# Kernel optimization log

Measured on AMD Instinct MI355X. Metric: run time of the kernel, lower is better.

## Reference

```python
import jax, jax.numpy as jnp
import numpy as np

N_STATE = 1280
N_HEAD = 20
D_HEAD = N_STATE // N_HEAD  # 64
N_MLP = 4 * N_STATE         # 5120
EPS = 1e-5


def _layer_norm(x, gamma, beta):
    mu = jnp.mean(x, axis=-1, keepdims=True)
    var = jnp.mean(jnp.square(x - mu), axis=-1, keepdims=True)
    return (x - mu) * jax.lax.rsqrt(var + EPS) * gamma + beta


def setup_inputs() -> dict:
    key = jax.random.key(0)
    ks = jax.random.split(key, 16)
    s = lambda fan_in: 1.0 / np.sqrt(fan_in)
    d = {
        "x": jax.random.normal(ks[0], (1, 1500, N_STATE), jnp.float32),
        # attention projections (stored [in, out]; torch Linear does x @ W.T + b)
        "Wq": jax.random.normal(ks[1], (N_STATE, N_STATE), jnp.float32) * s(N_STATE),
        "bq": jax.random.normal(ks[2], (N_STATE,), jnp.float32) * 0.02,
        "Wk": jax.random.normal(ks[3], (N_STATE, N_STATE), jnp.float32) * s(N_STATE),  # no bias
        "Wv": jax.random.normal(ks[4], (N_STATE, N_STATE), jnp.float32) * s(N_STATE),
        "bv": jax.random.normal(ks[5], (N_STATE,), jnp.float32) * 0.02,
        "Wo": jax.random.normal(ks[6], (N_STATE, N_STATE), jnp.float32) * s(N_STATE),
        "bo": jax.random.normal(ks[7], (N_STATE,), jnp.float32) * 0.02,
        # layer norms
        "ln1_g": jnp.ones((N_STATE,), jnp.float32),
        "ln1_b": jnp.zeros((N_STATE,), jnp.float32),
        "ln2_g": jnp.ones((N_STATE,), jnp.float32),
        "ln2_b": jnp.zeros((N_STATE,), jnp.float32),
        # MLP
        "W1": jax.random.normal(ks[8], (N_STATE, N_MLP), jnp.float32) * s(N_STATE),
        "b1": jax.random.normal(ks[9], (N_MLP,), jnp.float32) * 0.02,
        "W2": jax.random.normal(ks[10], (N_MLP, N_STATE), jnp.float32) * s(N_MLP),
        "b2": jax.random.normal(ks[11], (N_STATE,), jnp.float32) * 0.02,
    }
    return d


def reference(x, Wq, bq, Wk, Wv, bv, Wo, bo, ln1_g, ln1_b, ln2_g, ln2_b, W1, b1, W2, b2):
    B, S, C = x.shape
    scale = D_HEAD ** -0.5

    # --- multi-head self-attention ---
    h = _layer_norm(x, ln1_g, ln1_b)
    q = (h @ Wq + bq).reshape(B, S, N_HEAD, D_HEAD)
    k = (h @ Wk).reshape(B, S, N_HEAD, D_HEAD)
    v = (h @ Wv + bv).reshape(B, S, N_HEAD, D_HEAD)
    # scores: [B, H, Q, K]; softmax over keys (dim=1 'k' in the torch einsum)
    scores = jnp.einsum('bqhd,bkhd->bhqk', q, k) * scale
    w = jax.nn.softmax(scores, axis=-1)
    attn = jnp.einsum('bhqk,bkhd->bqhd', w, v).reshape(B, S, C)
    attn = attn @ Wo + bo
    x = x + attn

    # --- MLP (exact GELU, matching torch nn.GELU default) ---
    h2 = _layer_norm(x, ln2_g, ln2_b)
    h2 = jax.nn.gelu(h2 @ W1 + b1, approximate=False)
    x = x + (h2 @ W2 + b2)
    return x
```

## Files before the change

kernel.cpp:

```cpp
#include <hip/hip_runtime.h>
#include <hip/hip_bf16.h>
#include <math.h>

typedef __bf16 bf16x8 __attribute__((ext_vector_type(8)));
typedef float f32x4 __attribute__((ext_vector_type(4)));

#define SEQ 1500
#define CDIM 1280
#define NHEAD 20
#define DHEAD 64
#define NMLP 5120
#define QKVN 3840
#define VTLD 1504
#define APAD 68

#define GLOAD_LDS16(gp, lp)                                                    \
  __builtin_amdgcn_global_load_lds(                                            \
      (const __attribute__((address_space(1))) unsigned int*)(gp),             \
      (__attribute__((address_space(3))) unsigned int*)(lp), 16, 0, 0)

__global__ void detect_kernel(const unsigned int* __restrict__ xw,
                              int* __restrict__ flag) {
  __shared__ int cnt[256];
  const unsigned int w = xw[threadIdx.x];
  const unsigned int e = (w >> 7) & 0xFF;
  cnt[threadIdx.x] = (e >= 100 && e <= 150) ? 1 : 0;
  __syncthreads();
  for (int s = 128; s > 0; s >>= 1) {
    if (threadIdx.x < (unsigned)s) cnt[threadIdx.x] += cnt[threadIdx.x + s];
    __syncthreads();
  }
  if (threadIdx.x == 0) flag[0] = (cnt[0] >= 160) ? 1 : 0;
}

__global__ __launch_bounds__(256) void pack_params_kernel(
    const void* bq, const void* bv, const void* bo, const void* g1,
    const void* be1, const void* g2, const void* be2, const void* b1,
    const void* b2, __bf16* __restrict__ pb, const int* __restrict__ flag) {
  const int isbf = flag[0];
  const int i = blockIdx.x * 256 + threadIdx.x;
  if (i >= 16640) return;
  auto ld = [&](const void* p, int j) -> float {
    return isbf ? (float)((const __bf16*)p)[j] : ((const float*)p)[j];
  };
  float v;
  if (i < 3840) {
    if (i < 1280) v = ld(bq, i);
    else if (i < 2560) v = 0.f;
    else v = ld(bv, i - 2560);
  } else if (i < 5120) v = ld(bo, i - 3840);
  else if (i < 6400) v = ld(g1, i - 5120);
  else if (i < 7680) v = ld(be1, i - 6400);
  else if (i < 8960) v = ld(g2, i - 7680);
  else if (i < 10240) v = ld(be2, i - 8960);
  else if (i < 15360) v = ld(b1, i - 10240);
  else v = ld(b2, i - 15360);
  pb[i] = (__bf16)v;
}

__device__ __forceinline__ void transpose_body(const void* in, __bf16* out,
                                               int K, int N, int isbf) {
  __shared__ __bf16 t[32][33];
  const int tx = threadIdx.x, ty = threadIdx.y;
  const int n0 = blockIdx.x * 32, k0 = blockIdx.y * 32;
  if (isbf) {
    const __bf16* s = (const __bf16*)in;
#pragma unroll
    for (int i = ty; i < 32; i += 8)
      t[i][tx] = s[(size_t)(k0 + i) * N + n0 + tx];
  } else {
    const float* s = (const float*)in;
#pragma unroll
    for (int i = ty; i < 32; i += 8)
      t[i][tx] = (__bf16)s[(size_t)(k0 + i) * N + n0 + tx];
  }
  __syncthreads();
#pragma unroll
  for (int i = ty; i < 32; i += 8)
    out[(size_t)(n0 + i) * K + k0 + tx] = t[tx][i];
}

__global__ __launch_bounds__(256) void transpose_kernel(const void* __restrict__ in,
                                                        __bf16* __restrict__ out,
                                                        int K, int N,
                                                        const int* __restrict__ flag) {
  transpose_body(in, out, K, N, flag[0]);
}

__global__ __launch_bounds__(256) void transpose3_kernel(const void* __restrict__ Wq,
                                                         const void* __restrict__ Wk,
                                                         const void* __restrict__ Wv,
                                                         __bf16* __restrict__ out,
                                                         const int* __restrict__ flag) {
  const void* in = blockIdx.z == 0 ? Wq : (blockIdx.z == 1 ? Wk : Wv);
  transpose_body(in, out + (size_t)blockIdx.z * CDIM * CDIM, CDIM, CDIM, flag[0]);
}

__global__ __launch_bounds__(256) void transpose_act_kernel(const __bf16* __restrict__ in,
                                                            __bf16* __restrict__ out,
                                                            int istride) {
  __shared__ __bf16 t[32][33];
  const int tx = threadIdx.x, ty = threadIdx.y;
  const int n0 = blockIdx.x * 32, k0 = blockIdx.y * 32;
#pragma unroll
  for (int i = ty; i < 32; i += 8) {
    const int k = k0 + i;
    t[i][tx] = (k < SEQ) ? in[(size_t)k * istride + n0 + tx] : (__bf16)0.f;
  }
  __syncthreads();
#pragma unroll
  for (int i = ty; i < 32; i += 8) {
    const int kk = k0 + tx;
    if (kk < VTLD) out[(size_t)(n0 + i) * VTLD + kk] = t[tx][i];
  }
}

__global__ __launch_bounds__(256) void ln_kernel(const void* __restrict__ X,
                                                 const __bf16* __restrict__ gamma,
                                                 const __bf16* __restrict__ beta,
                                                 __bf16* __restrict__ Y,
                                                 int xflag, const int* __restrict__ flag) {
  const int isf32 = xflag ? (flag[0] == 0) : 0;
  const int row = blockIdx.x;
  float v[5];
  float s = 0.f, s2 = 0.f;
#pragma unroll
  for (int i = 0; i < 5; ++i) {
    const int c = threadIdx.x + 256 * i;
    const size_t idx = (size_t)row * CDIM + c;
    v[i] = isf32 ? ((const float*)X)[idx] : (float)((const __bf16*)X)[idx];
    s += v[i];
    s2 += v[i] * v[i];
  }
  const int lane = threadIdx.x & 63, wv = threadIdx.x >> 6;
#pragma unroll
  for (int off = 32; off > 0; off >>= 1) {
    s += __shfl_down(s, off);
    s2 += __shfl_down(s2, off);
  }
  __shared__ float red[8];
  if (lane == 0) { red[wv] = s; red[4 + wv] = s2; }
  __syncthreads();
  s = red[0] + red[1] + red[2] + red[3];
  s2 = red[4] + red[5] + red[6] + red[7];
  const float mu = s * (1.f / CDIM);
  const float var = s2 * (1.f / CDIM) - mu * mu;
  const float rstd = rsqrtf(fmaxf(var, 0.f) + 1e-5f);
#pragma unroll
  for (int i = 0; i < 5; ++i) {
    const int c = threadIdx.x + 256 * i;
    Y[(size_t)row * CDIM + c] =
        (__bf16)((v[i] - mu) * rstd * (float)gamma[c] + (float)beta[c]);
  }
}

__global__ __launch_bounds__(256) void gemm128s_kernel(
    const __bf16* __restrict__ A, const __bf16* __restrict__ Bt,
    const __bf16* __restrict__ bias, void* __restrict__ Cv,
    int M, int N, int K, int KS, int gelu, int nsplit,
    int mtiles, int ntpad) {
  __shared__ __bf16 As[2][2][128 * 32];
  __shared__ __bf16 Bs[2][2][128 * 32];

  int id = blockIdx.x;
  const int per = mtiles * ntpad;
  const int sz = id / per;
  id %= per;
  const int xcd = id & 7;
  const int grp = id >> 3;
  const int bm = grp % mtiles;
  const int bn = (grp / mtiles) * 8 + xcd;
  if (bn >= (N >> 7)) return;

  const int tid = threadIdx.x;
  const int lane = tid & 63, wave = tid >> 6;
  const int wm = (wave >> 1) * 64, wn = (wave & 1) * 64;
  const int l16 = lane & 15, kq = (lane >> 4) << 3;
  const int lrow = lane >> 2, lcol = (lane & 3) << 3;

  f32x4 acc[4][4];
  const f32x4 zero = {0.f, 0.f, 0.f, 0.f};
#pragma unroll
  for (int i = 0; i < 4; ++i)
#pragma unroll
    for (int j = 0; j < 4; ++j) acc[i][j] = zero;

  const __bf16* Ap[2];
  const __bf16* Bp[2];
#pragma unroll
  for (int t = 0; t < 2; ++t) {
    int ga = bm * 128 + t * 64 + wave * 16 + lrow;
    if (ga > M - 1) ga = M - 1;
    Ap[t] = A + (size_t)ga * K + lcol;
    const int gb = bn * 128 + t * 64 + wave * 16 + lrow;
    Bp[t] = Bt + (size_t)gb * K + lcol;
  }

  const int kbeg = sz * KS;
  int kend = kbeg + KS;
  if (kend > K) kend = K;

  auto stage = [&](int b, int k0) {
#pragma unroll
    for (int t = 0; t < 2; ++t)
#pragma unroll
      for (int c = 0; c < 2; ++c) {
        GLOAD_LDS16(Ap[t] + k0 + c * 32, &As[b][c][(t * 64 + wave * 16) * 32]);
        GLOAD_LDS16(Bp[t] + k0 + c * 32, &Bs[b][c][(t * 64 + wave * 16) * 32]);
      }
  };

  stage(0, kbeg);
  int buf = 0;
  for (int k0 = kbeg; k0 < kend; k0 += 64) {
    __syncthreads();
    if (k0 + 64 < kend) stage(buf ^ 1, k0 + 64);
    bf16x8 af[4][2], bfr[4][2];
#pragma unroll
    for (int i = 0; i < 4; ++i)
#pragma unroll
      for (int c = 0; c < 2; ++c)
        af[i][c] = *(const bf16x8*)(&As[buf][c][(wm + i * 16 + l16) * 32 + kq]);
#pragma unroll
    for (int j = 0; j < 4; ++j)
#pragma unroll
      for (int c = 0; c < 2; ++c)
        bfr[j][c] = *(const bf16x8*)(&Bs[buf][c][(wn + j * 16 + l16) * 32 + kq]);
#pragma unroll
    for (int i = 0; i < 4; ++i)
#pragma unroll
      for (int j = 0; j < 4; ++j)
#pragma unroll
        for (int c = 0; c < 2; ++c)
          acc[i][j] = __builtin_amdgcn_mfma_f32_16x16x32_bf16(af[i][c], bfr[j][c],
                                                              acc[i][j], 0, 0, 0);
    buf ^= 1;
  }

  const int rq4 = (lane >> 4) * 4;
  if (nsplit > 1) {
    float* P = (float*)Cv + (size_t)sz * M * N;
#pragma unroll
    for (int i = 0; i < 4; ++i)
#pragma unroll
      for (int r = 0; r < 4; ++r) {
        const int grow = bm * 128 + wm + i * 16 + rq4 + r;
        if (grow >= M) continue;
#pragma unroll
        for (int j = 0; j < 4; ++j) {
          const int gcol = bn * 128 + wn + j * 16 + l16;
          P[(size_t)grow * N + gcol] = acc[i][j][r];
        }
      }
  } else {
    __bf16* Cb = (__bf16*)Cv;
#pragma unroll
    for (int i = 0; i < 4; ++i)
#pragma unroll
      for (int r = 0; r < 4; ++r) {
        const int grow = bm * 128 + wm + i * 16 + rq4 + r;
        if (grow >= M) continue;
#pragma unroll
        for (int j = 0; j < 4; ++j) {
          const int gcol = bn * 128 + wn + j * 16 + l16;
          float vv = acc[i][j][r];
          if (bias) vv += (float)bias[gcol];
          if (gelu) vv = 0.5f * vv * (1.f + erff(vv * 0.70710678118654752f));
          Cb[(size_t)grow * N + gcol] = (__bf16)vv;
        }
      }
  }
}

__global__ __launch_bounds__(256) void reduce_kernel(
    const float* __restrict__ P, const __bf16* __restrict__ bias,
    const void* __restrict__ resid, void* __restrict__ out,
    int MN, int N, int S, int residflagged, int outflagged,
    const int* __restrict__ flag) {
  const int i = blockIdx.x * 256 + threadIdx.x;
  if (i >= MN) return;
  float v = 0.f;
  for (int s = 0; s < S; ++s) v += P[(size_t)s * MN + i];
  v += (float)bias[i % N];
  if (resid) {
    const int rf32 = residflagged ? (flag[0] == 0) : 0;
    v += rf32 ? ((const float*)resid)[i] : (float)((const __bf16*)resid)[i];
  }
  const int outbf = outflagged ? flag[0] : 1;
  if (outbf) ((__bf16*)out)[i] = (__bf16)v;
  else       ((float*)out)[i] = v;
}

__global__ __launch_bounds__(256) void attn_mfma_kernel(
    const __bf16* __restrict__ Q,
    const __bf16* __restrict__ Kk,
    const __bf16* __restrict__ Vt,
    float* __restrict__ Opart,
    float* __restrict__ ml,
    int rs) {
  const int h = blockIdx.y;
  const int q0 = blockIdx.x * 64;
  const int z = blockIdx.z;
  const int tid = threadIdx.x;
  const int wave = tid >> 6, lane = tid & 63;
  const int l16 = lane & 15, quad = lane >> 4;

  __shared__ __bf16 Ks[64 * APAD];
  __shared__ __bf16 Vs[64 * APAD];
  __shared__ __bf16 Ps[4][16 * APAD];

  bf16x8 qf[2];
  {
    int q = q0 + wave * 16 + l16;
    if (q > SEQ - 1) q = SEQ - 1;
    const __bf16* qp = Q + (size_t)q * rs + h * DHEAD + quad * 8;
    qf[0] = *(const bf16x8*)(qp);
    qf[1] = *(const bf16x8*)(qp + 32);
  }

  f32x4 oacc[4];
  const f32x4 zero = {0.f, 0.f, 0.f, 0.f};
#pragma unroll
  for (int jt = 0; jt < 4; ++jt) oacc[jt] = zero;
  float mrow[4], lrow[4];
#pragma unroll
  for (int r = 0; r < 4; ++r) { mrow[r] = -30000.f; lrow[r] = 0.f; }

  const int srow = tid >> 2;
  const int scol = (tid & 3) << 4;

  const __bf16* Kbase = Kk + h * DHEAD;
  const __bf16* Vbase = Vt + (size_t)(h * DHEAD + srow) * VTLD;

  for (int kt = z * 12; kt < z * 12 + 12; ++kt) {
    const int key0 = kt * 64;
    __syncthreads();
    {
      int gk = key0 + srow;
      if (gk > SEQ - 1) gk = SEQ - 1;
      const __bf16* kp = Kbase + (size_t)gk * rs + scol;
      *(bf16x8*)(&Ks[srow * APAD + scol]) = *(const bf16x8*)(kp);
      *(bf16x8*)(&Ks[srow * APAD + scol + 8]) = *(const bf16x8*)(kp + 8);
      const __bf16* vp = Vbase + key0 + scol;
      *(bf16x8*)(&Vs[srow * APAD + scol]) = *(const bf16x8*)(vp);
      *(bf16x8*)(&Vs[srow * APAD + scol + 8]) = *(const bf16x8*)(vp + 8);
    }
    __syncthreads();

    f32x4 s[4];
#pragma unroll
    for (int jt = 0; jt < 4; ++jt) s[jt] = zero;
#pragma unroll
    for (int jt = 0; jt < 4; ++jt)
#pragma unroll
      for (int ks = 0; ks < 2; ++ks) {
        const bf16x8 kf = *(const bf16x8*)(&Ks[(jt * 16 + l16) * APAD + ks * 32 + quad * 8]);
        s[jt] = __builtin_amdgcn_mfma_f32_16x16x32_bf16(qf[ks], kf, s[jt], 0, 0, 0);
      }

#pragma unroll
    for (int jt = 0; jt < 4; ++jt) {
      const int key = key0 + jt * 16 + l16;
#pragma unroll
      for (int r = 0; r < 4; ++r) {
        float sv = s[jt][r] * 0.125f;
        if (key >= SEQ) sv = -30000.f;
        s[jt][r] = sv;
      }
    }

#pragma unroll
    for (int r = 0; r < 4; ++r) {
      float tmax = fmaxf(fmaxf(s[0][r], s[1][r]), fmaxf(s[2][r], s[3][r]));
#pragma unroll
      for (int off = 8; off > 0; off >>= 1) tmax = fmaxf(tmax, __shfl_xor(tmax, off));
      const float mnew = fmaxf(mrow[r], tmax);
      const float alpha = __expf(mrow[r] - mnew);
      mrow[r] = mnew;
      lrow[r] *= alpha;
#pragma unroll
      for (int jt = 0; jt < 4; ++jt) oacc[jt][r] *= alpha;
#pragma unroll
      for (int jt = 0; jt < 4; ++jt) {
        const float p = __expf(s[jt][r] - mnew);
        lrow[r] += p;
        Ps[wave][(quad * 4 + r) * APAD + jt * 16 + l16] = (__bf16)p;
      }
    }

    bf16x8 pf[2];
    pf[0] = *(const bf16x8*)(&Ps[wave][l16 * APAD + quad * 8]);
    pf[1] = *(const bf16x8*)(&Ps[wave][l16 * APAD + 32 + quad * 8]);
#pragma unroll
    for (int jt = 0; jt < 4; ++jt)
#pragma unroll
      for (int ks = 0; ks < 2; ++ks) {
        const bf16x8 vf = *(const bf16x8*)(&Vs[(jt * 16 + l16) * APAD + ks * 32 + quad * 8]);
        oacc[jt] = __builtin_amdgcn_mfma_f32_16x16x32_bf16(pf[ks], vf, oacc[jt], 0, 0, 0);
      }
  }

  float* Oz = Opart + (size_t)z * SEQ * CDIM;
#pragma unroll
  for (int r = 0; r < 4; ++r) {
    float lt = lrow[r];
#pragma unroll
    for (int off = 8; off > 0; off >>= 1) lt += __shfl_xor(lt, off);
    const int q = q0 + wave * 16 + quad * 4 + r;
    if (q < SEQ) {
#pragma unroll
      for (int jt = 0; jt < 4; ++jt)
        Oz[(size_t)q * CDIM + h * DHEAD + jt * 16 + l16] = oacc[jt][r];
      if (l16 == 0) {
        const size_t mi = ((size_t)(z * NHEAD + h) * SEQ + q) * 2;
        ml[mi] = mrow[r];
        ml[mi + 1] = lt;
      }
    }
  }
}

__global__ __launch_bounds__(256) void attn_combine_kernel(
    const float* __restrict__ Op, const float* __restrict__ ml,
    __bf16* __restrict__ O) {
  const int i = blockIdx.x * 256 + threadIdx.x;
  if (i >= SEQ * CDIM) return;
  const int q = i / CDIM;
  const int h = (i % CDIM) >> 6;
  const size_t m1i = ((size_t)h * SEQ + q) * 2;
  const size_t m2i = ((size_t)(NHEAD + h) * SEQ + q) * 2;
  const float m1 = ml[m1i], l1 = ml[m1i + 1];
  const float m2 = ml[m2i], l2 = ml[m2i + 1];
  const float M = fmaxf(m1, m2);
  const float e1 = __expf(m1 - M), e2 = __expf(m2 - M);
  const float v = (e1 * Op[i] + e2 * Op[(size_t)SEQ * CDIM + i]) /
                  (e1 * l1 + e2 * l2);
  O[i] = (__bf16)v;
}

extern "C" void kernel_launch(void* const* d_in, const int* in_sizes, int n_in,
                              void* d_out, int out_size, void* d_ws, size_t ws_size,
                              hipStream_t stream) {
  const void* x   = d_in[0];
  const void* Wq  = d_in[1];
  const void* bq  = d_in[2];
  const void* Wk  = d_in[3];
  const void* Wv  = d_in[4];
  const void* bv  = d_in[5];
  const void* Wo  = d_in[6];
  const void* bo  = d_in[7];
  const void* g1  = d_in[8];
  const void* be1 = d_in[9];
  const void* g2  = d_in[10];
  const void* be2 = d_in[11];
  const void* W1  = d_in[12];
  const void* bm1 = d_in[13];
  const void* W2  = d_in[14];
  const void* bm2 = d_in[15];

  char* ws = (char*)d_ws;
  size_t off = 0;
  auto alloc = [&](size_t elems) {
    __bf16* p = (__bf16*)(ws + off);
    off += elems * sizeof(__bf16);
    return p;
  };
  __bf16* Wqkvt = alloc((size_t)QKVN * CDIM);
  __bf16* Wot   = alloc((size_t)CDIM * CDIM);
  __bf16* W1t   = alloc((size_t)CDIM * NMLP);
  __bf16* W2t   = alloc((size_t)CDIM * NMLP);
  __bf16* qkvb  = alloc((size_t)SEQ * QKVN);
  __bf16* hb    = alloc((size_t)SEQ * CDIM);
  __bf16* mb    = alloc((size_t)SEQ * NMLP);
  __bf16* pb    = alloc(20480);
  off = (off + 15) & ~(size_t)15;
  float* pscr = (float*)(ws + off);
  off += (size_t)2 * SEQ * CDIM * sizeof(float);
  float* mlb = (float*)(ws + off);
  off += (size_t)2 * NHEAD * SEQ * 2 * sizeof(float);
  int* flag = (int*)(ws + off);

  __bf16* vtb  = mb;
  __bf16* x1b  = qkvb;
  __bf16* h2b  = qkvb + (size_t)SEQ * CDIM;

  __bf16* qkvbias = pb + 0;
  __bf16* bo_b  = pb + 3840;
  __bf16* g1_b  = pb + 5120;
  __bf16* be1_b = pb + 6400;
  __bf16* g2_b  = pb + 7680;
  __bf16* be2_b = pb + 8960;
  __bf16* b1_b  = pb + 10240;
  __bf16* b2_b  = pb + 15360;

  detect_kernel<<<1, 256, 0, stream>>>((const unsigned int*)x, flag);
  pack_params_kernel<<<65, 256, 0, stream>>>(bq, bv, bo, g1, be1, g2, be2,
                                             bm1, bm2, pb, flag);

  const dim3 tb(32, 8);
  transpose3_kernel<<<dim3(40, 40, 3), tb, 0, stream>>>(Wq, Wk, Wv, Wqkvt, flag);
  transpose_kernel<<<dim3(40, 40), tb, 0, stream>>>(Wo, Wot, CDIM, CDIM, flag);
  transpose_kernel<<<dim3(160, 40), tb, 0, stream>>>(W1, W1t, CDIM, NMLP, flag);
  transpose_kernel<<<dim3(40, 160), tb, 0, stream>>>(W2, W2t, NMLP, CDIM, flag);

  ln_kernel<<<SEQ, 256, 0, stream>>>(x, g1_b, be1_b, hb, 1, flag);
  gemm128s_kernel<<<12 * 32, 256, 0, stream>>>(
      hb, Wqkvt, qkvbias, qkvb, SEQ, QKVN, CDIM, CDIM, 0, 1, 12, 32);
  transpose_act_kernel<<<dim3(40, 47), tb, 0, stream>>>(qkvb + 2560, vtb, QKVN);
  attn_mfma_kernel<<<dim3(24, NHEAD, 2), 256, 0, stream>>>(
      qkvb, qkvb + 1280, vtb, pscr, mlb, QKVN);
  attn_combine_kernel<<<7500, 256, 0, stream>>>(pscr, mlb, hb);
  gemm128s_kernel<<<12 * 16 * 2, 256, 0, stream>>>(
      hb, Wot, nullptr, pscr, SEQ, CDIM, CDIM, 640, 0, 2, 12, 16);
  reduce_kernel<<<7500, 256, 0, stream>>>(pscr, bo_b, x, x1b,
                                          SEQ * CDIM, CDIM, 2, 1, 0, flag);
  ln_kernel<<<SEQ, 256, 0, stream>>>(x1b, g2_b, be2_b, h2b, 0, flag);
  gemm128s_kernel<<<12 * 40, 256, 0, stream>>>(
      h2b, W1t, b1_b, mb, SEQ, NMLP, CDIM, CDIM, 1, 1, 12, 40);
  gemm128s_kernel<<<12 * 16 * 2, 256, 0, stream>>>(
      mb, W2t, nullptr, pscr, SEQ, CDIM, NMLP, 2560, 0, 2, 12, 16);
  reduce_kernel<<<7500, 256, 0, stream>>>(pscr, b2_b, x1b, d_out,
                                          SEQ * CDIM, CDIM, 2, 0, 1, flag);
}
```

Before: 395.3 us.

## Store GEMM operands in 128x32 tile-packed layout for contiguous LDS staging

Introduces a packed tile layout (128-row by 32-column blocks stored contiguously) for transposed weights, layernorm outputs, attention output and the MLP hidden activation, so each GEMM k-step stage is a single contiguous 16-byte-per-lane load into LDS. The GEMM now steps K by 32 with half the shared memory, and uses a plain 3D grid in place of the XCD-aware tile swizzle. The aim is to make global loads fully coalesced and simplify addressing. In exchange there are twice as many loop iterations and barriers, L2 locality from the XCD mapping is lost, and the packed buffers need padding to 1536 rows.

Measured after the change: 436.5 us. 10.4% more time.

```diff
diff --git a/kernel.cpp b/kernel.cpp
--- a/kernel.cpp
+++ b/kernel.cpp
@@ -13,6 +13,11 @@
 #define QKVN 3840
 #define VTLD 1504
 #define APAD 68
+
+__device__ __forceinline__ size_t pidx(int row, int col, int K) {
+  return (size_t)(row >> 7) * ((size_t)K * 128) + (size_t)(col >> 5) * 4096 +
+         (size_t)(row & 127) * 32 + (col & 31);
+}
 
 #define GLOAD_LDS16(gp, lp)                                                    \
   __builtin_amdgcn_global_load_lds(                                            \
@@ -77,7 +82,7 @@
   __syncthreads();
 #pragma unroll
   for (int i = ty; i < 32; i += 8)
-    out[(size_t)(n0 + i) * K + k0 + tx] = t[tx][i];
+    out[pidx(n0 + i, k0 + tx, K)] = t[tx][i];
 }
 
 __global__ __launch_bounds__(256) void transpose_kernel(const void* __restrict__ in,
@@ -149,34 +154,22 @@
 #pragma unroll
   for (int i = 0; i < 5; ++i) {
     const int c = threadIdx.x + 256 * i;
-    Y[(size_t)row * CDIM + c] =
+    Y[pidx(row, c, CDIM)] =
         (__bf16)((v[i] - mu) * rstd * (float)gamma[c] + (float)beta[c]);
   }
 }
 
-__global__ __launch_bounds__(256) void gemm128s_kernel(
+__global__ __launch_bounds__(256) void gemm_kernel(
     const __bf16* __restrict__ A, const __bf16* __restrict__ Bt,
     const __bf16* __restrict__ bias, void* __restrict__ Cv,
-    int M, int N, int K, int KS, int gelu, int nsplit,
-    int mtiles, int ntpad) {
-  __shared__ __bf16 As[2][2][128 * 32];
-  __shared__ __bf16 Bs[2][2][128 * 32];
-
-  int id = blockIdx.x;
-  const int per = mtiles * ntpad;
-  const int sz = id / per;
-  id %= per;
-  const int xcd = id & 7;
-  const int grp = id >> 3;
-  const int bm = grp % mtiles;
-  const int bn = (grp / mtiles) * 8 + xcd;
-  if (bn >= (N >> 7)) return;
-
+    int M, int N, int K, int KS, int gelu, int nsplit, int packC) {
+  __shared__ __bf16 As[2][128 * 32];
+  __shared__ __bf16 Bs[2][128 * 32];
+  const int bm = blockIdx.x, bn = blockIdx.y, sz = blockIdx.z;
   const int tid = threadIdx.x;
   const int lane = tid & 63, wave = tid >> 6;
   const int wm = (wave >> 1) * 64, wn = (wave & 1) * 64;
   const int l16 = lane & 15, kq = (lane >> 4) << 3;
-  const int lrow = lane >> 2, lcol = (lane & 3) << 3;
 
   f32x4 acc[4][4];
   const f32x4 zero = {0.f, 0.f, 0.f, 0.f};
@@ -185,55 +178,41 @@
 #pragma unroll
     for (int j = 0; j < 4; ++j) acc[i][j] = zero;
 
-  const __bf16* Ap[2];
-  const __bf16* Bp[2];
-#pragma unroll
-  for (int t = 0; t < 2; ++t) {
-    int ga = bm * 128 + t * 64 + wave * 16 + lrow;
-    if (ga > M - 1) ga = M - 1;
-    Ap[t] = A + (size_t)ga * K + lcol;
-    const int gb = bn * 128 + t * 64 + wave * 16 + lrow;
-    Bp[t] = Bt + (size_t)gb * K + lcol;
-  }
+  const __bf16* Apk = A + (size_t)bm * K * 128 + lane * 8;
+  const __bf16* Bpk = Bt + (size_t)bn * K * 128 + lane * 8;
 
   const int kbeg = sz * KS;
   int kend = kbeg + KS;
   if (kend > K) kend = K;
 
   auto stage = [&](int b, int k0) {
-#pragma unroll
-    for (int t = 0; t < 2; ++t)
-#pragma unroll
-      for (int c = 0; c < 2; ++c) {
-        GLOAD_LDS16(Ap[t] + k0 + c * 32, &As[b][c][(t * 64 + wave * 16) * 32]);
-        GLOAD_LDS16(Bp[t] + k0 + c * 32, &Bs[b][c][(t * 64 + wave * 16) * 32]);
-      }
+    const size_t co = (size_t)(k0 >> 5) * 4096;
+#pragma unroll
+    for (int t = 0; t < 2; ++t) {
+      const int seg = (t * 64 + wave * 16) * 32;
+      GLOAD_LDS16(Apk + co + seg, &As[b][seg]);
+      GLOAD_LDS16(Bpk + co + seg, &Bs[b][seg]);
+    }
   };
 
   stage(0, kbeg);
   int buf = 0;
-  for (int k0 = kbeg; k0 < kend; k0 += 64) {
+  for (int k0 = kbeg; k0 < kend; k0 += 32) {
     __syncthreads();
-    if (k0 + 64 < kend) stage(buf ^ 1, k0 + 64);
-    bf16x8 af[4][2], bfr[4][2];
+    if (k0 + 32 < kend) stage(buf ^ 1, k0 + 32);
+    bf16x8 af[4], bfr[4];
 #pragma unroll
     for (int i = 0; i < 4; ++i)
-#pragma unroll
-      for (int c = 0; c < 2; ++c)
-        af[i][c] = *(const bf16x8*)(&As[buf][c][(wm + i * 16 + l16) * 32 + kq]);
+      af[i] = *(const bf16x8*)(&As[buf][(wm + i * 16 + l16) * 32 + kq]);
 #pragma unroll
     for (int j = 0; j < 4; ++j)
-#pragma unroll
-      for (int c = 0; c < 2; ++c)
-        bfr[j][c] = *(const bf16x8*)(&Bs[buf][c][(wn + j * 16 + l16) * 32 + kq]);
+      bfr[j] = *(const bf16x8*)(&Bs[buf][(wn + j * 16 + l16) * 32 + kq]);
 #pragma unroll
     for (int i = 0; i < 4; ++i)
 #pragma unroll
       for (int j = 0; j < 4; ++j)
-#pragma unroll
-        for (int c = 0; c < 2; ++c)
-          acc[i][j] = __builtin_amdgcn_mfma_f32_16x16x32_bf16(af[i][c], bfr[j][c],
-                                                              acc[i][j], 0, 0, 0);
+        acc[i][j] = __builtin_amdgcn_mfma_f32_16x16x32_bf16(af[i], bfr[j],
+                                                            acc[i][j], 0, 0, 0);
     buf ^= 1;
   }
 
@@ -266,7 +245,8 @@
           float vv = acc[i][j][r];
           if (bias) vv += (float)bias[gcol];
           if (gelu) vv = 0.5f * vv * (1.f + erff(vv * 0.70710678118654752f));
-          Cb[(size_t)grow * N + gcol] = (__bf16)vv;
+          if (packC) Cb[pidx(grow, gcol, N)] = (__bf16)vv;
+          else       Cb[(size_t)grow * N + gcol] = (__bf16)vv;
         }
       }
   }
@@ -426,7 +406,8 @@
   const int i = blockIdx.x * 256 + threadIdx.x;
   if (i >= SEQ * CDIM) return;
   const int q = i / CDIM;
-  const int h = (i % CDIM) >> 6;
+  const int c = i % CDIM;
+  const int h = c >> 6;
   const size_t m1i = ((size_t)h * SEQ + q) * 2;
   const size_t m2i = ((size_t)(NHEAD + h) * SEQ + q) * 2;
   const float m1 = ml[m1i], l1 = ml[m1i + 1];
@@ -435,7 +416,7 @@
   const float e1 = __expf(m1 - M), e2 = __expf(m2 - M);
   const float v = (e1 * Op[i] + e2 * Op[(size_t)SEQ * CDIM + i]) /
                   (e1 * l1 + e2 * l2);
-  O[i] = (__bf16)v;
+  O[pidx(q, c, CDIM)] = (__bf16)v;
 }
 
 extern "C" void kernel_launch(void* const* d_in, const int* in_sizes, int n_in,
@@ -470,8 +451,8 @@
   __bf16* W1t   = alloc((size_t)CDIM * NMLP);
   __bf16* W2t   = alloc((size_t)CDIM * NMLP);
   __bf16* qkvb  = alloc((size_t)SEQ * QKVN);
-  __bf16* hb    = alloc((size_t)SEQ * CDIM);
-  __bf16* mb    = alloc((size_t)SEQ * NMLP);
+  __bf16* hb    = alloc((size_t)12 * 128 * CDIM);
+  __bf16* mb    = alloc((size_t)12 * 128 * NMLP);
   __bf16* pb    = alloc(20480);
   off = (off + 15) & ~(size_t)15;
   float* pscr = (float*)(ws + off);
@@ -482,7 +463,7 @@
 
   __bf16* vtb  = mb;
   __bf16* x1b  = qkvb;
-  __bf16* h2b  = qkvb + (size_t)SEQ * CDIM;
+  __bf16* h2b  = qkvb + (size_t)2097152;
 
   __bf16* qkvbias = pb + 0;
   __bf16* bo_b  = pb + 3840;
@@ -504,21 +485,21 @@
   transpose_kernel<<<dim3(40, 160), tb, 0, stream>>>(W2, W2t, NMLP, CDIM, flag);
 
   ln_kernel<<<SEQ, 256, 0, stream>>>(x, g1_b, be1_b, hb, 1, flag);
-  gemm128s_kernel<<<12 * 32, 256, 0, stream>>>(
-      hb, Wqkvt, qkvbias, qkvb, SEQ, QKVN, CDIM, CDIM, 0, 1, 12, 32);
+  gemm_kernel<<<dim3(12, 30, 1), 256, 0, stream>>>(
+      hb, Wqkvt, qkvbias, qkvb, SEQ, QKVN, CDIM, CDIM, 0, 1, 0);
   transpose_act_kernel<<<dim3(40, 47), tb, 0, stream>>>(qkvb + 2560, vtb, QKVN);
   attn_mfma_kernel<<<dim3(24, NHEAD, 2), 256, 0, stream>>>(
       qkvb, qkvb + 1280, vtb, pscr, mlb, QKVN);
   attn_combine_kernel<<<7500, 256, 0, stream>>>(pscr, mlb, hb);
-  gemm128s_kernel<<<12 * 16 * 2, 256, 0, stream>>>(
-      hb, Wot, nullptr, pscr, SEQ, CDIM, CDIM, 640, 0, 2, 12, 16);
+  gemm_kernel<<<dim3(12, 10, 2), 256, 0, stream>>>(
+      hb, Wot, nullptr, pscr, SEQ, CDIM, CDIM, 640, 0, 2, 0);
   reduce_kernel<<<7500, 256, 0, stream>>>(pscr, bo_b, x, x1b,
                                           SEQ * CDIM, CDIM, 2, 1, 0, flag);
   ln_kernel<<<SEQ, 256, 0, stream>>>(x1b, g2_b, be2_b, h2b, 0, flag);
-  gemm128s_kernel<<<12 * 40, 256, 0, stream>>>(
-      h2b, W1t, b1_b, mb, SEQ, NMLP, CDIM, CDIM, 1, 1, 12, 40);
-  gemm128s_kernel<<<12 * 16 * 2, 256, 0, stream>>>(
-      mb, W2t, nullptr, pscr, SEQ, CDIM, NMLP, 2560, 0, 2, 12, 16);
+  gemm_kernel<<<dim3(12, 40, 1), 256, 0, stream>>>(
+      h2b, W1t, b1_b, mb, SEQ, NMLP, CDIM, CDIM, 1, 1, 1);
+  gemm_kernel<<<dim3(12, 10, 2), 256, 0, stream>>>(
+      mb, W2t, nullptr, pscr, SEQ, CDIM, NMLP, 2560, 0, 2, 0);
   reduce_kernel<<<7500, 256, 0, stream>>>(pscr, b2_b, x1b, d_out,
                                           SEQ * CDIM, CDIM, 2, 0, 1, flag);
 }
```
